# Kernel optimization log

Measured on AMD Instinct MI355X. Metric: run time of the kernel, lower is better.

## Reference

```python
import jax, jax.numpy as jnp
import numpy as np

N = 100000   # nodes
E = 1600000  # edges
D_IN, D_H, D_OUT = 128, 128, 64
BN_EPS = 1e-5


def setup_inputs() -> dict:
    key = jax.random.key(0)
    ks = jax.random.split(key, 12)

    def lin_w(k, fan_in, shape):
        s = 1.0 / np.sqrt(fan_in)
        return jax.random.uniform(k, shape, jnp.float32, -s, s)

    return {
        "x": jax.random.normal(ks[0], (N, D_IN), jnp.float32),
        "edge_index": jax.random.randint(ks[1], (2, E), 0, N, dtype=jnp.int64),
        "edge_weight": jax.random.uniform(ks[2], (E,), jnp.float32),
        "W1": lin_w(ks[3], D_IN, (D_IN, D_H)),
        "b1": jnp.zeros((D_H,), jnp.float32),
        "W2": lin_w(ks[4], D_H, (D_H, D_H)),
        "b2": jnp.zeros((D_H,), jnp.float32),
        "W3": lin_w(ks[5], D_H, (D_H, D_OUT)),
        "b3": jnp.zeros((D_OUT,), jnp.float32),
        "gamma1": jnp.ones((D_H,), jnp.float32),
        "beta1": jnp.zeros((D_H,), jnp.float32),
        "gamma2": jnp.ones((D_H,), jnp.float32),
        "beta2": jnp.zeros((D_H,), jnp.float32),
    }


def _gcn_conv(x, src, dst, w, W, b):
    # PyG GCNConv: x' = D^{-1/2} (A + I) D^{-1/2} (x W) + b, self-loop weight 1
    n = x.shape[0]
    h = x @ W                                   # [N, d_out]
    loop = jnp.arange(n, dtype=src.dtype)
    s = jnp.concatenate([src, loop])            # [E+N]
    d = jnp.concatenate([dst, loop])
    ww = jnp.concatenate([w, jnp.ones((n,), w.dtype)])
    deg = jax.ops.segment_sum(ww, d, num_segments=n)          # in-degree at targets
    dinv = jnp.where(deg > 0, jax.lax.rsqrt(deg), 0.0)
    norm = dinv[s] * ww * dinv[d]               # [E+N]
    msg = h[s] * norm[:, None]                  # gather + scale
    out = jax.ops.segment_sum(msg, d, num_segments=n)
    return out + b


def _batch_norm(x, gamma, beta):
    mean = jnp.mean(x, axis=0)
    var = jnp.mean(jnp.square(x - mean), axis=0)  # biased, as BatchNorm uses
    return (x - mean) * jax.lax.rsqrt(var + BN_EPS) * gamma + beta


def reference(x, edge_index, edge_weight, W1, b1, W2, b2, W3, b3,
              gamma1, beta1, gamma2, beta2):
    src, dst = edge_index[0], edge_index[1]
    h = _gcn_conv(x, src, dst, edge_weight, W1, b1)
    h = jax.nn.relu(_batch_norm(h, gamma1, beta1))
    h = _gcn_conv(h, src, dst, edge_weight, W2, b2)
    h = jax.nn.relu(_batch_norm(h, gamma2, beta2))
    return _gcn_conv(h, src, dst, edge_weight, W3, b3)
```

## Files before the change

kernel.cpp:

```cpp
#include <hip/hip_runtime.h>
#include <hip/hip_fp16.h>
#include <cstdint>
#include <cstddef>

#define BN_EPS 1e-5f
#define FPSCALE 268435456.0f
#define M40 0xFFFFFFFFFFULL

typedef _Float16 half8 __attribute__((ext_vector_type(8)));
typedef float floatx4 __attribute__((ext_vector_type(4)));

__device__ __forceinline__ float wn_of(unsigned v) {
    __half_raw hr; hr.x = (unsigned short)(v & 0x7fffu);
    return __half2float((__half)hr);
}

static __device__ __forceinline__ int load_edge(const void* ei, int mode64, long long pos) {
    if (mode64) return (int)((const long long*)ei)[pos];
    return ((const int*)ei)[pos];
}

__device__ __forceinline__ float dinv_of(unsigned long long p) {
    return rsqrtf(1.0f + (float)(p & M40) * (1.0f / FPSCALE));
}

__global__ __launch_bounds__(256) void init_kernel(const unsigned* __restrict__ eiw, int nwords,
                                                   int* __restrict__ mode,
                                                   unsigned long long* __restrict__ packed, int N,
                                                   const float* __restrict__ W1,
                                                   const float* __restrict__ W2,
                                                   const float* __restrict__ W3,
                                                   _Float16* __restrict__ WT1,
                                                   _Float16* __restrict__ WT2,
                                                   _Float16* __restrict__ WT3, int nb) {
    __shared__ unsigned red[256];
    const int bid = (int)blockIdx.x;
    const int tid = (int)threadIdx.x;
    if (bid < nb) {
        int i = bid * 256 + tid;
        if (i < N) packed[i] = 0ULL;
        return;
    }
    if (bid == nb) {
        unsigned m = 0;
        for (int i = 1 + 2 * tid; i < nwords; i += 512) m |= eiw[i];
        red[tid] = m;
        __syncthreads();
        for (int s = 128; s > 0; s >>= 1) {
            if (tid < s) red[tid] |= red[tid + s];
            __syncthreads();
        }
        if (tid == 0) mode[0] = (red[0] == 0) ? 1 : 0;
        return;
    }
    const int t_ = bid - nb - 1;
    if (t_ < 64) {
        int t = t_ * 256 + tid;
        int n = t / 128, k = t % 128;
        WT1[t] = (_Float16)W1[k * 128 + n];
    } else if (t_ < 128) {
        int t = (t_ - 64) * 256 + tid;
        int n = t / 128, k = t % 128;
        WT2[t] = (_Float16)W2[k * 128 + n];
    } else {
        int t = (t_ - 128) * 256 + tid;
        int n = t / 128, k = t % 128;
        WT3[t] = (_Float16)W3[k * 64 + n];
    }
}

template <int M, bool BN, typename TI>
__device__ __forceinline__ void gemm_body(int gbid, const TI* __restrict__ X,
                                          const _Float16* __restrict__ WTg,
                                          const float* __restrict__ sc,
                                          const float* __restrict__ sh,
                                          __half* __restrict__ Hout, int N,
                                          _Float16* WT ) {
    constexpr int CT = M / 16;
    constexpr int LDK = 136;

    for (int t = threadIdx.x; t < M * 16; t += 256) {
        int n = t / 16, seg = t % 16;
        *(half8*)&WT[n * LDK + seg * 8] = *(const half8*)&WTg[n * 128 + seg * 8];
    }
    __syncthreads();

    const int wave = (int)threadIdx.x >> 6;
    const int lane = (int)threadIdx.x & 63;
    const int qd = lane >> 4;
    const int ln = lane & 15;
    const int tile0 = gbid * 64 + wave * 16;
    int ar = tile0 + ln;
    if (ar >= N) ar = N - 1;

    half8 aF[4];
    const TI* xr = X + (size_t)ar * 128 + qd * 8;
#pragma unroll
    for (int kb = 0; kb < 4; ++kb) {
        float vv[8];
        if constexpr (sizeof(TI) == 4) {
            float4 v0 = *(const float4*)(xr + kb * 32);
            float4 v1 = *(const float4*)(xr + kb * 32 + 4);
            vv[0] = v0.x; vv[1] = v0.y; vv[2] = v0.z; vv[3] = v0.w;
            vv[4] = v1.x; vv[5] = v1.y; vv[6] = v1.z; vv[7] = v1.w;
        } else {
            half8 raw = *(const half8*)(xr + kb * 32);
#pragma unroll
            for (int j = 0; j < 8; ++j) vv[j] = (float)raw[j];
        }
        if (BN) {
            const int kbase = kb * 32 + qd * 8;
#pragma unroll
            for (int j = 0; j < 8; ++j)
                vv[j] = fmaxf(fmaf(vv[j], sc[kbase + j], sh[kbase + j]), 0.0f);
        }
        half8 a;
#pragma unroll
        for (int j = 0; j < 8; ++j) a[j] = (_Float16)vv[j];
        aF[kb] = a;
    }

#pragma unroll
    for (int ct = 0; ct < CT; ++ct) {
        floatx4 acc = {0.0f, 0.0f, 0.0f, 0.0f};
#pragma unroll
        for (int kb = 0; kb < 4; ++kb) {
            half8 b = *(const half8*)&WT[(ct * 16 + ln) * LDK + kb * 32 + qd * 8];
            acc = __builtin_amdgcn_mfma_f32_16x16x32_f16(aF[kb], b, acc, 0, 0, 0);
        }
#pragma unroll
        for (int r = 0; r < 4; ++r) {
            int orow = tile0 + qd * 4 + r;
            if (orow < N) Hout[(size_t)orow * M + ct * 16 + ln] = __float2half(acc[r]);
        }
    }
}

__global__ __launch_bounds__(256) void hist_gemm1_kernel(const void* __restrict__ ei,
                                                         const float* __restrict__ ew,
                                                         unsigned long long* __restrict__ packed,
                                                         unsigned* __restrict__ slot32,
                                                         const int* __restrict__ mode, int E, int GB,
                                                         const float* __restrict__ X,
                                                         const _Float16* __restrict__ WT1g,
                                                         __half* __restrict__ Hout, int N) {
    __shared__ _Float16 WT[128 * 136];
    if ((int)blockIdx.x < GB) {
        gemm_body<128, false, float>(blockIdx.x, X, WT1g, nullptr, nullptr, Hout, N, WT);
        return;
    }
    int e = ((int)blockIdx.x - GB) * 256 + (int)threadIdx.x;
    if (e >= E) return;
    int md = *mode;
    int d = load_edge(ei, md, (long long)E + e);
    unsigned long long contrib = (1ULL << 40) | (unsigned long long)(ew[e] * FPSCALE);
    unsigned long long old = atomicAdd(&packed[d], contrib);
    unsigned r = (unsigned)(old >> 40);
    slot32[e] = ((unsigned)d << 6) | (r < 63u ? r : 63u);
}

__global__ __launch_bounds__(256) void scatter_zero_kernel(const void* __restrict__ ei,
                                                           const float* __restrict__ ew,
                                                           const unsigned long long* __restrict__ packed,
                                                           const unsigned* __restrict__ slot32,
                                                           unsigned* __restrict__ edata,
                                                           const int* __restrict__ mode, int E, int EBK,
                                                           float* __restrict__ gsum,
                                                           float* __restrict__ gsq,
                                                           int* __restrict__ tickets) {
    if ((int)blockIdx.x == EBK) {
        if (threadIdx.x < 128) { gsum[threadIdx.x] = 0.0f; gsq[threadIdx.x] = 0.0f; }
        if (threadIdx.x < 2) tickets[threadIdx.x] = 0;
        return;
    }
    int e = (int)blockIdx.x * 256 + (int)threadIdx.x;
    if (e >= E) return;
    int md = *mode;
    int s = load_edge(ei, md, e);
    unsigned sl = slot32[e];
    int d = (int)(sl >> 6);
    float wn = dinv_of(packed[s]) * ew[e] * dinv_of(packed[d]);
    unsigned hb = (unsigned)__half_as_ushort(__float2half(wn)) & 0x7fffu;
    edata[sl] = ((unsigned)s << 15) | hb;
}

template <int D, bool BIAS, typename TY>
__global__ __launch_bounds__(256) void agg_kernel(const __half* __restrict__ H,
                                                  const unsigned* __restrict__ edata,
                                                  const unsigned long long* __restrict__ packed,
                                                  const float* __restrict__ bias,
                                                  TY* __restrict__ Y, int N) {
    constexpr int LPR = D / 8;
    constexpr int GROUPS = 64 / LPR;
    const int lane = (int)threadIdx.x & 63;
    const int i = (int)blockIdx.x * 4 + ((int)threadIdx.x >> 6);
    if (i >= N) return;
    const int g = lane / LPR;
    const int c0 = (lane % LPR) * 8;

    const unsigned long long p = packed[i];
    int n = (int)(p >> 40);
    n = n < 64 ? n : 64;
    const float di = dinv_of(p);

    unsigned ev = 0;
    if (lane < n) ev = edata[((size_t)i << 6) + lane];

    float acc[8] = {};
    for (int j = 0; j < n; j += 4 * GROUPS) {
        const unsigned e0 = __shfl(ev, j + g);
        const unsigned e1 = __shfl(ev, j + GROUPS + g);
        const unsigned e2 = __shfl(ev, j + 2 * GROUPS + g);
        const unsigned e3 = __shfl(ev, j + 3 * GROUPS + g);
        const half8 h0 = *(const half8*)(H + (size_t)(e0 >> 15) * D + c0);
        const half8 h1 = *(const half8*)(H + (size_t)(e1 >> 15) * D + c0);
        const half8 h2 = *(const half8*)(H + (size_t)(e2 >> 15) * D + c0);
        const half8 h3 = *(const half8*)(H + (size_t)(e3 >> 15) * D + c0);
        const float w0 = wn_of(e0), w1 = wn_of(e1), w2 = wn_of(e2), w3 = wn_of(e3);
#pragma unroll
        for (int k = 0; k < 8; ++k) acc[k] = fmaf(w0, (float)h0[k], acc[k]);
#pragma unroll
        for (int k = 0; k < 8; ++k) acc[k] = fmaf(w1, (float)h1[k], acc[k]);
#pragma unroll
        for (int k = 0; k < 8; ++k) acc[k] = fmaf(w2, (float)h2[k], acc[k]);
#pragma unroll
        for (int k = 0; k < 8; ++k) acc[k] = fmaf(w3, (float)h3[k], acc[k]);
    }

#pragma unroll
    for (int m = LPR; m < 64; m <<= 1) {
#pragma unroll
        for (int k = 0; k < 8; ++k) acc[k] += __shfl_xor(acc[k], m);
    }

    if (lane < LPR) {
        const float dii = di * di;
        const half8 hs = *(const half8*)(H + (size_t)i * D + c0);
#pragma unroll
        for (int k = 0; k < 8; ++k) acc[k] = fmaf(dii, (float)hs[k], acc[k]);
        if (BIAS) {
#pragma unroll
            for (int k = 0; k < 8; ++k) acc[k] += bias[c0 + k];
        }
        if constexpr (sizeof(TY) == 2) {
            half8 o;
#pragma unroll
            for (int k = 0; k < 8; ++k) o[k] = (_Float16)acc[k];
            *(half8*)((__half*)Y + (size_t)i * D + c0) = o;
        } else {
            float4 o0 = make_float4(acc[0], acc[1], acc[2], acc[3]);
            float4 o1 = make_float4(acc[4], acc[5], acc[6], acc[7]);
            *(float4*)((float*)Y + (size_t)i * D + c0) = o0;
            *(float4*)((float*)Y + (size_t)i * D + c0 + 4) = o1;
        }
    }
}

template <int M, bool BN, typename TI, bool ZERO>
__global__ __launch_bounds__(256) void gemm_mfma_kernel(const TI* __restrict__ X,
                                                        const _Float16* __restrict__ WTg,
                                                        const float* __restrict__ sc,
                                                        const float* __restrict__ sh,
                                                        __half* __restrict__ Hout, int N,
                                                        float* __restrict__ gsum,
                                                        float* __restrict__ gsq, int GB) {
    __shared__ _Float16 WT[M * 136];
    if (ZERO && (int)blockIdx.x == GB) {
        if (threadIdx.x < 128) { gsum[threadIdx.x] = 0.0f; gsq[threadIdx.x] = 0.0f; }
        return;
    }
    gemm_body<M, BN, TI>(blockIdx.x, X, WTg, sc, sh, Hout, N, WT);
}

__global__ __launch_bounds__(256) void stats_fin_kernel(const __half* __restrict__ Y,
                                                        float* __restrict__ gsum,
                                                        float* __restrict__ gsq, int N,
                                                        int* __restrict__ ticket,
                                                        const float* __restrict__ gamma,
                                                        const float* __restrict__ beta,
                                                        float* __restrict__ sc,
                                                        float* __restrict__ sh) {
    __shared__ float ls[256], lq[256];
    __shared__ int isLast;
    const int tid = (int)threadIdx.x;
    const int c = tid & 127;
    const int half_ = tid >> 7;
    float s = 0.0f, q = 0.0f;
    for (int row = (int)blockIdx.x * 2 + half_; row < N; row += 512) {
        float v = __half2float(Y[(size_t)row * 128 + c]);
        s += v;
        q = fmaf(v, v, q);
    }
    ls[tid] = s; lq[tid] = q;
    __syncthreads();
    if (tid < 128) {
        atomicAdd(&gsum[c], ls[tid] + ls[tid + 128]);
        atomicAdd(&gsq[c],  lq[tid] + lq[tid + 128]);
    }
    __threadfence();
    __syncthreads();
    if (tid == 0) {
        int old = atomicAdd(ticket, 1);
        isLast = (old == (int)gridDim.x - 1);
    }
    __syncthreads();
    if (isLast && tid < 128) {
        float gs = __hip_atomic_load(&gsum[tid], __ATOMIC_RELAXED, __HIP_MEMORY_SCOPE_AGENT);
        float gq = __hip_atomic_load(&gsq[tid],  __ATOMIC_RELAXED, __HIP_MEMORY_SCOPE_AGENT);
        float inv_n = 1.0f / (float)N;
        float mean = gs * inv_n;
        float var = gq * inv_n - mean * mean;
        float scale = gamma[tid] * rsqrtf(var + BN_EPS);
        sc[tid] = scale;
        sh[tid] = beta[tid] - mean * scale;
    }
}

extern "C" void kernel_launch(void* const* d_in, const int* in_sizes, int n_in,
                              void* d_out, int out_size, void* d_ws, size_t ws_size,
                              hipStream_t stream) {
    const float* x   = (const float*)d_in[0];
    const void*  ei  = d_in[1];
    const float* ew  = (const float*)d_in[2];
    const float* W1  = (const float*)d_in[3];
    const float* W2  = (const float*)d_in[5];
    const float* W3  = (const float*)d_in[7];
    const float* b3  = (const float*)d_in[8];
    const float* g1  = (const float*)d_in[9];
    const float* be1 = (const float*)d_in[10];
    const float* g2  = (const float*)d_in[11];
    const float* be2 = (const float*)d_in[12];
    float* out = (float*)d_out;

    const int N = in_sizes[0] / 128;
    const int E = in_sizes[2];

    char* w = (char*)d_ws;
    size_t off = 0;
    auto alloc = [&](size_t bytes) -> void* {
        void* p = w + off;
        off += (bytes + 255) & ~(size_t)255;
        return p;
    };
    unsigned long long* packed = (unsigned long long*)alloc((size_t)N * 8);
    unsigned* slot32 = (unsigned*)alloc((size_t)E * 4);
    unsigned* edata  = (unsigned*)alloc((size_t)N * 64 * 4);
    int*   mode      = (int*)  alloc(256);
    int*   tickets   = (int*)  alloc(256);
    float* gsum      = (float*)alloc(128 * 4);
    float* gsq       = (float*)alloc(128 * 4);
    float* scb       = (float*)alloc(128 * 4);
    float* shb       = (float*)alloc(128 * 4);
    _Float16* WT1    = (_Float16*)alloc(128 * 128 * 2);
    _Float16* WT2    = (_Float16*)alloc(128 * 128 * 2);
    _Float16* WT3    = (_Float16*)alloc(128 * 64 * 2);
    __half* H        = (__half*)alloc((size_t)N * 128 * 2);
    __half* Yh       = (__half*)alloc((size_t)N * 128 * 2);
    (void)ws_size; (void)n_in; (void)out_size;

    const int nb  = (N + 255) / 256;
    const int ebk = (E + 255) / 256;
    const int gb  = (N + 63) / 64;
    const int ab  = (N + 3) / 4;

    init_kernel<<<nb + 1 + 160, 256, 0, stream>>>((const unsigned*)ei, 4096, mode, packed, N,
                                                  W1, W2, W3, WT1, WT2, WT3, nb);
    hist_gemm1_kernel<<<gb + ebk, 256, 0, stream>>>(ei, ew, packed, slot32, mode, E, gb,
                                                    x, WT1, H, N);
    scatter_zero_kernel<<<ebk + 1, 256, 0, stream>>>(ei, ew, packed, slot32, edata,
                                                     mode, E, ebk, gsum, gsq, tickets);

    agg_kernel<128, false, __half><<<ab, 256, 0, stream>>>(H, edata, packed, nullptr, Yh, N);
    stats_fin_kernel<<<256, 256, 0, stream>>>(Yh, gsum, gsq, N, &tickets[0], g1, be1, scb, shb);

    gemm_mfma_kernel<128, true, __half, true><<<gb + 1, 256, 0, stream>>>(Yh, WT2, scb, shb, H, N, gsum, gsq, gb);
    agg_kernel<128, false, __half><<<ab, 256, 0, stream>>>(H, edata, packed, nullptr, Yh, N);
    stats_fin_kernel<<<256, 256, 0, stream>>>(Yh, gsum, gsq, N, &tickets[1], g2, be2, scb, shb);

    gemm_mfma_kernel<64, true, __half, false><<<gb, 256, 0, stream>>>(Yh, WT3, scb, shb, H, N, nullptr, nullptr, gb);
    agg_kernel<64, true, float><<<ab, 256, 0, stream>>>(H, edata, packed, b3, out, N);
}
```

Baseline: 560.6 us.

## Drop scatter kernel by writing raw edge weights and folding normalization into GEMM

Removes the separate scatter_zero pass. The histogram kernel now writes the CSR-like edge slots directly, holding raw edge weights instead of fully normalized ones. The D^{-1/2} factors are split: the source-side factor is applied in the GEMM epilogue (layers 2 and 3) or per edge in layer-1 aggregation, and the destination factor is applied once per row at the end of aggregation. This saves one edge pass and the slot32 buffer, at the cost of extra packed[] gathers in the first aggregation and a different fp16 rounding of the weights.

```diff
diff --git a/kernel.cpp b/kernel.cpp
--- a/kernel.cpp
+++ b/kernel.cpp
@@ -32,7 +32,10 @@
                                                    const float* __restrict__ W3,
                                                    _Float16* __restrict__ WT1,
                                                    _Float16* __restrict__ WT2,
-                                                   _Float16* __restrict__ WT3, int nb) {
+                                                   _Float16* __restrict__ WT3, int nb,
+                                                   float* __restrict__ gsum,
+                                                   float* __restrict__ gsq,
+                                                   int* __restrict__ tickets) {
     __shared__ unsigned red[256];
     const int bid = (int)blockIdx.x;
     const int tid = (int)threadIdx.x;
@@ -42,6 +45,8 @@
         return;
     }
     if (bid == nb) {
+        if (tid < 128) { gsum[tid] = 0.0f; gsq[tid] = 0.0f; }
+        if (tid < 2) tickets[tid] = 0;
         unsigned m = 0;
         for (int i = 1 + 2 * tid; i < nwords; i += 512) m |= eiw[i];
         red[tid] = m;
@@ -69,11 +74,12 @@
     }
 }
 
-template <int M, bool BN, typename TI>
+template <int M, bool BN, typename TI, bool SCALE_OUT>
 __device__ __forceinline__ void gemm_body(int gbid, const TI* __restrict__ X,
                                           const _Float16* __restrict__ WTg,
                                           const float* __restrict__ sc,
                                           const float* __restrict__ sh,
+                                          const unsigned long long* __restrict__ packed,
                                           __half* __restrict__ Hout, int N,
                                           _Float16* WT ) {
     constexpr int CT = M / 16;
@@ -120,6 +126,15 @@
         aF[kb] = a;
     }
 
+    float dv[4];
+    if constexpr (SCALE_OUT) {
+#pragma unroll
+        for (int r = 0; r < 4; ++r) {
+            int orow = tile0 + qd * 4 + r;
+            dv[r] = dinv_of(packed[orow < N ? orow : 0]);
+        }
+    }
+
 #pragma unroll
     for (int ct = 0; ct < CT; ++ct) {
         floatx4 acc = {0.0f, 0.0f, 0.0f, 0.0f};
@@ -131,7 +146,9 @@
 #pragma unroll
         for (int r = 0; r < 4; ++r) {
             int orow = tile0 + qd * 4 + r;
-            if (orow < N) Hout[(size_t)orow * M + ct * 16 + ln] = __float2half(acc[r]);
+            float o = acc[r];
+            if constexpr (SCALE_OUT) o *= dv[r];
+            if (orow < N) Hout[(size_t)orow * M + ct * 16 + ln] = __float2half(o);
         }
     }
 }
@@ -139,52 +156,31 @@
 __global__ __launch_bounds__(256) void hist_gemm1_kernel(const void* __restrict__ ei,
                                                          const float* __restrict__ ew,
                                                          unsigned long long* __restrict__ packed,
-                                                         unsigned* __restrict__ slot32,
+                                                         unsigned* __restrict__ edata,
                                                          const int* __restrict__ mode, int E, int GB,
                                                          const float* __restrict__ X,
                                                          const _Float16* __restrict__ WT1g,
                                                          __half* __restrict__ Hout, int N) {
     __shared__ _Float16 WT[128 * 136];
     if ((int)blockIdx.x < GB) {
-        gemm_body<128, false, float>(blockIdx.x, X, WT1g, nullptr, nullptr, Hout, N, WT);
+        gemm_body<128, false, float, false>(blockIdx.x, X, WT1g, nullptr, nullptr, nullptr, Hout, N, WT);
         return;
     }
     int e = ((int)blockIdx.x - GB) * 256 + (int)threadIdx.x;
     if (e >= E) return;
     int md = *mode;
+    int s = load_edge(ei, md, e);
     int d = load_edge(ei, md, (long long)E + e);
-    unsigned long long contrib = (1ULL << 40) | (unsigned long long)(ew[e] * FPSCALE);
+    float w = ew[e];
+    unsigned long long contrib = (1ULL << 40) | (unsigned long long)(w * FPSCALE);
     unsigned long long old = atomicAdd(&packed[d], contrib);
     unsigned r = (unsigned)(old >> 40);
-    slot32[e] = ((unsigned)d << 6) | (r < 63u ? r : 63u);
-}
-
-__global__ __launch_bounds__(256) void scatter_zero_kernel(const void* __restrict__ ei,
-                                                           const float* __restrict__ ew,
-                                                           const unsigned long long* __restrict__ packed,
-                                                           const unsigned* __restrict__ slot32,
-                                                           unsigned* __restrict__ edata,
-                                                           const int* __restrict__ mode, int E, int EBK,
-                                                           float* __restrict__ gsum,
-                                                           float* __restrict__ gsq,
-                                                           int* __restrict__ tickets) {
-    if ((int)blockIdx.x == EBK) {
-        if (threadIdx.x < 128) { gsum[threadIdx.x] = 0.0f; gsq[threadIdx.x] = 0.0f; }
-        if (threadIdx.x < 2) tickets[threadIdx.x] = 0;
-        return;
-    }
-    int e = (int)blockIdx.x * 256 + (int)threadIdx.x;
-    if (e >= E) return;
-    int md = *mode;
-    int s = load_edge(ei, md, e);
-    unsigned sl = slot32[e];
-    int d = (int)(sl >> 6);
-    float wn = dinv_of(packed[s]) * ew[e] * dinv_of(packed[d]);
-    unsigned hb = (unsigned)__half_as_ushort(__float2half(wn)) & 0x7fffu;
-    edata[sl] = ((unsigned)s << 15) | hb;
-}
-
-template <int D, bool BIAS, typename TY>
+    r = r < 63u ? r : 63u;
+    unsigned hb = (unsigned)__half_as_ushort(__float2half(w)) & 0x7fffu;
+    edata[((size_t)d << 6) | r] = ((unsigned)s << 15) | hb;
+}
+
+template <int D, bool BIAS, bool SCALED, typename TY>
 __global__ __launch_bounds__(256) void agg_kernel(const __half* __restrict__ H,
                                                   const unsigned* __restrict__ edata,
                                                   const unsigned long long* __restrict__ packed,
@@ -216,7 +212,13 @@
         const half8 h1 = *(const half8*)(H + (size_t)(e1 >> 15) * D + c0);
         const half8 h2 = *(const half8*)(H + (size_t)(e2 >> 15) * D + c0);
         const half8 h3 = *(const half8*)(H + (size_t)(e3 >> 15) * D + c0);
-        const float w0 = wn_of(e0), w1 = wn_of(e1), w2 = wn_of(e2), w3 = wn_of(e3);
+        float w0 = wn_of(e0), w1 = wn_of(e1), w2 = wn_of(e2), w3 = wn_of(e3);
+        if constexpr (!SCALED) {
+            w0 *= dinv_of(packed[e0 >> 15]);
+            w1 *= dinv_of(packed[e1 >> 15]);
+            w2 *= dinv_of(packed[e2 >> 15]);
+            w3 *= dinv_of(packed[e3 >> 15]);
+        }
 #pragma unroll
         for (int k = 0; k < 8; ++k) acc[k] = fmaf(w0, (float)h0[k], acc[k]);
 #pragma unroll
@@ -234,10 +236,12 @@
     }
 
     if (lane < LPR) {
-        const float dii = di * di;
+        const float selfw = SCALED ? 1.0f : di;
         const half8 hs = *(const half8*)(H + (size_t)i * D + c0);
 #pragma unroll
-        for (int k = 0; k < 8; ++k) acc[k] = fmaf(dii, (float)hs[k], acc[k]);
+        for (int k = 0; k < 8; ++k) acc[k] = fmaf(selfw, (float)hs[k], acc[k]);
+#pragma unroll
+        for (int k = 0; k < 8; ++k) acc[k] *= di;
         if (BIAS) {
 #pragma unroll
             for (int k = 0; k < 8; ++k) acc[k] += bias[c0 + k];
@@ -261,6 +265,7 @@
                                                         const _Float16* __restrict__ WTg,
                                                         const float* __restrict__ sc,
                                                         const float* __restrict__ sh,
+                                                        const unsigned long long* __restrict__ packed,
                                                         __half* __restrict__ Hout, int N,
                                                         float* __restrict__ gsum,
                                                         float* __restrict__ gsq, int GB) {
@@ -269,7 +274,7 @@
         if (threadIdx.x < 128) { gsum[threadIdx.x] = 0.0f; gsq[threadIdx.x] = 0.0f; }
         return;
     }
-    gemm_body<M, BN, TI>(blockIdx.x, X, WTg, sc, sh, Hout, N, WT);
+    gemm_body<M, BN, TI, true>(blockIdx.x, X, WTg, sc, sh, packed, Hout, N, WT);
 }
 
 __global__ __launch_bounds__(256) void stats_fin_kernel(const __half* __restrict__ Y,
@@ -343,7 +348,6 @@
         return p;
     };
     unsigned long long* packed = (unsigned long long*)alloc((size_t)N * 8);
-    unsigned* slot32 = (unsigned*)alloc((size_t)E * 4);
     unsigned* edata  = (unsigned*)alloc((size_t)N * 64 * 4);
     int*   mode      = (int*)  alloc(256);
     int*   tickets   = (int*)  alloc(256);
@@ -364,19 +368,18 @@
     const int ab  = (N + 3) / 4;
 
     init_kernel<<<nb + 1 + 160, 256, 0, stream>>>((const unsigned*)ei, 4096, mode, packed, N,
-                                                  W1, W2, W3, WT1, WT2, WT3, nb);
-    hist_gemm1_kernel<<<gb + ebk, 256, 0, stream>>>(ei, ew, packed, slot32, mode, E, gb,
+                                                  W1, W2, W3, WT1, WT2, WT3, nb,
+                                                  gsum, gsq, tickets);
+    hist_gemm1_kernel<<<gb + ebk, 256, 0, stream>>>(ei, ew, packed, edata, mode, E, gb,
                                                     x, WT1, H, N);
-    scatter_zero_kernel<<<ebk + 1, 256, 0, stream>>>(ei, ew, packed, slot32, edata,
-                                                     mode, E, ebk, gsum, gsq, tickets);
-
-    agg_kernel<128, false, __half><<<ab, 256, 0, stream>>>(H, edata, packed, nullptr, Yh, N);
+
+    agg_kernel<128, false, false, __half><<<ab, 256, 0, stream>>>(H, edata, packed, nullptr, Yh, N);
     stats_fin_kernel<<<256, 256, 0, stream>>>(Yh, gsum, gsq, N, &tickets[0], g1, be1, scb, shb);
 
-    gemm_mfma_kernel<128, true, __half, true><<<gb + 1, 256, 0, stream>>>(Yh, WT2, scb, shb, H, N, gsum, gsq, gb);
-    agg_kernel<128, false, __half><<<ab, 256, 0, stream>>>(H, edata, packed, nullptr, Yh, N);
+    gemm_mfma_kernel<128, true, __half, true><<<gb + 1, 256, 0, stream>>>(Yh, WT2, scb, shb, packed, H, N, gsum, gsq, gb);
+    agg_kernel<128, false, true, __half><<<ab, 256, 0, stream>>>(H, edata, packed, nullptr, Yh, N);
     stats_fin_kernel<<<256, 256, 0, stream>>>(Yh, gsum, gsq, N, &tickets[1], g2, be2, scb, shb);
 
-    gemm_mfma_kernel<64, true, __half, false><<<gb, 256, 0, stream>>>(Yh, WT3, scb, shb, H, N, nullptr, nullptr, gb);
-    agg_kernel<64, true, float><<<ab, 256, 0, stream>>>(H, edata, packed, b3, out, N);
-}
+    gemm_mfma_kernel<64, true, __half, false><<<gb, 256, 0, stream>>>(Yh, WT3, scb, shb, packed, H, N, nullptr, nullptr, gb);
+    agg_kernel<64, true, true, float><<<ab, 256, 0, stream>>>(H, edata, packed, b3, out, N);
+}
```

Result: no change. 571.9 us (+2.0%).
